# Kernel optimization log

Hardware: AMD Instinct MI355X
Metric: run time of the kernel (lower is better)

Reference implementation:

```python
import jax, jax.numpy as jnp
import numpy as np

NUM_HEADS = 16
LN_EPS = 1e-5


def setup_inputs() -> dict:
    key = jax.random.key(0)
    ks = jax.random.split(key, 5)
    B, S, H = 32768, 3, 1024
    scale = 1.0 / np.sqrt(H)
    return {
        "slots": jax.random.normal(ks[0], (B, S, H), dtype=jnp.float32),
        "in_proj_w": jax.random.normal(ks[1], (3 * H, H), dtype=jnp.float32) * scale,
        "in_proj_b": jax.random.normal(ks[2], (3 * H,), dtype=jnp.float32) * 0.02,
        "out_w": jax.random.normal(ks[3], (H, H), dtype=jnp.float32) * scale,
        "out_b": jax.random.normal(ks[4], (H,), dtype=jnp.float32) * 0.02,
        "ln_g": jnp.ones((H,), dtype=jnp.float32),
        "ln_b": jnp.zeros((H,), dtype=jnp.float32),
    }


def reference(slots, in_proj_w, in_proj_b, out_w, out_b, ln_g, ln_b):
    # slots: [B, 3, H]. Matches torch nn.MultiheadAttention (batch_first) in eval
    # mode (dropout inactive) followed by residual add + LayerNorm.
    B, S, H = slots.shape
    nh = NUM_HEADS
    dh = H // nh

    # fused QKV projection: torch does x @ in_proj_w.T + in_proj_b
    qkv = jnp.einsum("bsh,eh->bse", slots, in_proj_w) + in_proj_b  # [B,S,3H]
    q, k, v = jnp.split(qkv, 3, axis=-1)

    def heads(t):  # [B,S,H] -> [B,nh,S,dh]
        return t.reshape(B, S, nh, dh).transpose(0, 2, 1, 3)

    q, k, v = heads(q), heads(k), heads(v)

    scores = jnp.einsum("bnqd,bnkd->bnqk", q, k) / jnp.sqrt(jnp.asarray(dh, slots.dtype))
    attn = jax.nn.softmax(scores, axis=-1)  # [B,nh,3,3]
    ctx = jnp.einsum("bnqk,bnkd->bnqd", attn, v)  # [B,nh,3,dh]
    ctx = ctx.transpose(0, 2, 1, 3).reshape(B, S, H)

    attn_out = jnp.einsum("bsh,oh->bso", ctx, out_w) + out_b  # out_proj

    # residual + LayerNorm (dropout is identity at inference)
    y = slots + attn_out
    mu = jnp.mean(y, axis=-1, keepdims=True)
    var = jnp.mean(jnp.square(y - mu), axis=-1, keepdims=True)
    return (y - mu) / jnp.sqrt(var + LN_EPS) * ln_g + ln_b
```

## Files before the change

### kernel.cpp

```cpp
#include <hip/hip_runtime.h>
#include <stdint.h>

typedef unsigned short u16;
typedef float f32x4 __attribute__((ext_vector_type(4)));
typedef short bf16x8 __attribute__((ext_vector_type(8)));

__device__ __forceinline__ u16 f2bu(float f) {
  uint32_t x = __builtin_bit_cast(uint32_t, f);
  x += 0x7fffu + ((x >> 16) & 1u);
  return (u16)(x >> 16);
}
__device__ __forceinline__ float b2f(u16 u) {
  return __builtin_bit_cast(float, (uint32_t)u << 16);
}
__device__ __forceinline__ void gll16(const void* g, void* l) {
  __builtin_amdgcn_global_load_lds(
      (const __attribute__((address_space(1))) void*)g,
      (__attribute__((address_space(3))) void*)l, 16, 0, 0);
}
#define MEMFENCE asm volatile("" ::: "memory")
#define BAR() do { __builtin_amdgcn_s_barrier(); MEMFENCE; } while (0)

__global__ __launch_bounds__(256) void cvt_f32_bf16_kernel(
    const float* __restrict__ in, u16* __restrict__ out, int n4) {
  int i = blockIdx.x * 256 + threadIdx.x;
  const int stride = gridDim.x * 256;
  for (; i < n4; i += stride) {
    float4 f = reinterpret_cast<const float4*>(in)[i];
    ushort4 o;
    o.x = f2bu(f.x); o.y = f2bu(f.y); o.z = f2bu(f.z); o.w = f2bu(f.w);
    reinterpret_cast<ushort4*>(out)[i] = o;
  }
}

__global__ __launch_bounds__(512, 2) void gemm256_bt_bias(
    const u16* __restrict__ A, const u16* __restrict__ Bw,
    const float* __restrict__ bias, u16* __restrict__ C,
    int N, int K, int ntn) {
  __shared__ u16 lds[2][2][2][8192];
  const int tid = threadIdx.x;
  const int lane = tid & 63, wid = tid >> 6;
  const int wr = wid >> 2, wc = wid & 3;
  const int fr = lane & 15, kg = lane >> 4;

  const int cpx = (int)gridDim.x >> 3;
  const int bid = blockIdx.x;
  const int sid = (bid & 7) * cpx + (bid >> 3);
  const int mt = sid / ntn, nt = sid % ntn;

  const int srow = tid >> 2;
  const int scol = (tid & 3) ^ ((tid >> 3) & 3);
  const u16* Ag = A + (size_t)(mt * 256 + srow) * K + scol * 8;
  const u16* Bg = Bw + (size_t)(nt * 256 + srow) * K + scol * 8;
  const size_t rstep = (size_t)128 * K;

  const int sw = (fr >> 1) & 3;
  const int kgs = (kg ^ sw) * 8;
  const int aoff = (wr * 128 + fr) * 32 + kgs;
  const int boff = (wc * 64 + fr) * 32 + kgs;

  f32x4 acc[8][4];
#pragma unroll
  for (int i = 0; i < 8; i++)
#pragma unroll
    for (int j = 0; j < 4; j++) acc[i][j] = f32x4{0.f, 0.f, 0.f, 0.f};

  const int NT = K >> 6;

#define STAGE_A(kh, kt, nb) do {                               \
    const u16* s_ = Ag + (size_t)(kt) * 64 + (kh) * 32;        \
    gll16(s_,         &lds[nb][0][kh][wid * 512]);             \
    gll16(s_ + rstep, &lds[nb][0][kh][4096 + wid * 512]);      \
  } while (0)
#define STAGE_B(kh, kt, nb) do {                               \
    const u16* s_ = Bg + (size_t)(kt) * 64 + (kh) * 32;        \
    gll16(s_,         &lds[nb][1][kh][wid * 512]);             \
    gll16(s_ + rstep, &lds[nb][1][kh][4096 + wid * 512]);      \
  } while (0)

  STAGE_A(0, 0, 0); STAGE_B(0, 0, 0);
  STAGE_A(1, 0, 0); STAGE_B(1, 0, 0);
  asm volatile("s_waitcnt vmcnt(4)" ::: "memory");
  BAR();

  for (int t = 0; t < NT; t++) {
    const int buf = t & 1, nb = buf ^ 1;
    const bool st = (t + 1 < NT);
    const u16* As0 = &lds[buf][0][0][0];
    const u16* As1 = &lds[buf][0][1][0];
    const u16* Bs0 = &lds[buf][1][0][0];
    const u16* Bs1 = &lds[buf][1][1][0];

    bf16x8 av[8], bv[2];

#pragma unroll
    for (int mi = 0; mi < 8; mi++)
      av[mi] = *(const bf16x8*)&As0[aoff + mi * 512];
    bv[0] = *(const bf16x8*)&Bs0[boff];
    bv[1] = *(const bf16x8*)&Bs0[boff + 512];
    if (st) STAGE_A(0, t + 1, nb);
    BAR();
    __builtin_amdgcn_s_setprio(1);
#pragma unroll
    for (int mi = 0; mi < 8; mi++) {
      acc[mi][0] = __builtin_amdgcn_mfma_f32_16x16x32_bf16(av[mi], bv[0], acc[mi][0], 0, 0, 0);
      acc[mi][1] = __builtin_amdgcn_mfma_f32_16x16x32_bf16(av[mi], bv[1], acc[mi][1], 0, 0, 0);
    }
    __builtin_amdgcn_s_setprio(0);
    BAR();

    bv[0] = *(const bf16x8*)&Bs0[boff + 1024];
    bv[1] = *(const bf16x8*)&Bs0[boff + 1536];
    if (st) STAGE_B(0, t + 1, nb);
    BAR();
    __builtin_amdgcn_s_setprio(1);
#pragma unroll
    for (int mi = 0; mi < 8; mi++) {
      acc[mi][2] = __builtin_amdgcn_mfma_f32_16x16x32_bf16(av[mi], bv[0], acc[mi][2], 0, 0, 0);
      acc[mi][3] = __builtin_amdgcn_mfma_f32_16x16x32_bf16(av[mi], bv[1], acc[mi][3], 0, 0, 0);
    }
    __builtin_amdgcn_s_setprio(0);
    if (t == NT - 1) asm volatile("s_waitcnt vmcnt(0)" ::: "memory");
    else             asm volatile("s_waitcnt vmcnt(4)" ::: "memory");
    BAR();

#pragma unroll
    for (int mi = 0; mi < 8; mi++)
      av[mi] = *(const bf16x8*)&As1[aoff + mi * 512];
    bv[0] = *(const bf16x8*)&Bs1[boff];
    bv[1] = *(const bf16x8*)&Bs1[boff + 512];
    if (st) STAGE_A(1, t + 1, nb);
    BAR();
    __builtin_amdgcn_s_setprio(1);
#pragma unroll
    for (int mi = 0; mi < 8; mi++) {
      acc[mi][0] = __builtin_amdgcn_mfma_f32_16x16x32_bf16(av[mi], bv[0], acc[mi][0], 0, 0, 0);
      acc[mi][1] = __builtin_amdgcn_mfma_f32_16x16x32_bf16(av[mi], bv[1], acc[mi][1], 0, 0, 0);
    }
    __builtin_amdgcn_s_setprio(0);
    BAR();

    bv[0] = *(const bf16x8*)&Bs1[boff + 1024];
    bv[1] = *(const bf16x8*)&Bs1[boff + 1536];
    if (st) STAGE_B(1, t + 1, nb);
    BAR();
    __builtin_amdgcn_s_setprio(1);
#pragma unroll
    for (int mi = 0; mi < 8; mi++) {
      acc[mi][2] = __builtin_amdgcn_mfma_f32_16x16x32_bf16(av[mi], bv[0], acc[mi][2], 0, 0, 0);
      acc[mi][3] = __builtin_amdgcn_mfma_f32_16x16x32_bf16(av[mi], bv[1], acc[mi][3], 0, 0, 0);
    }
    __builtin_amdgcn_s_setprio(0);
    asm volatile("s_waitcnt vmcnt(4)" ::: "memory");
    BAR();
  }
#undef STAGE_A
#undef STAGE_B

  const int crow0 = mt * 256 + wr * 128 + kg * 4;
  const int ccol0 = nt * 256 + wc * 64 + fr;
#pragma unroll
  for (int nj = 0; nj < 4; nj++) {
    const int col = ccol0 + nj * 16;
    const float bb = bias[col];
#pragma unroll
    for (int mi = 0; mi < 8; mi++) {
      const int r0 = crow0 + mi * 16;
      f32x4 v = acc[mi][nj];
#pragma unroll
      for (int r = 0; r < 4; r++)
        C[(size_t)(r0 + r) * N + col] = f2bu(v[r] + bb);
    }
  }
}

__global__ __launch_bounds__(256) void attn3_kernel(
    const u16* __restrict__ qkv, u16* __restrict__ ctx) {
  const int tid = threadIdx.x;
  const int lane = tid & 63, wid = tid >> 6;
  const int unit = blockIdx.x * 4 + wid;
  const int b = unit >> 2, hg = unit & 3;
  const size_t qbase = (size_t)b * 3 * 3072 + hg * 256 + lane * 4;

  float q[3][4], k[3][4], v[3][4];
#pragma unroll
  for (int s = 0; s < 3; s++) {
    ushort4 uq = *(const ushort4*)(qkv + qbase + (size_t)s * 3072);
    ushort4 uk = *(const ushort4*)(qkv + qbase + (size_t)s * 3072 + 1024);
    ushort4 uv = *(const ushort4*)(qkv + qbase + (size_t)s * 3072 + 2048);
    q[s][0] = b2f(uq.x); q[s][1] = b2f(uq.y); q[s][2] = b2f(uq.z); q[s][3] = b2f(uq.w);
    k[s][0] = b2f(uk.x); k[s][1] = b2f(uk.y); k[s][2] = b2f(uk.z); k[s][3] = b2f(uk.w);
    v[s][0] = b2f(uv.x); v[s][1] = b2f(uv.y); v[s][2] = b2f(uv.z); v[s][3] = b2f(uv.w);
  }

  float sc[3][3];
#pragma unroll
  for (int i = 0; i < 3; i++)
#pragma unroll
    for (int j = 0; j < 3; j++) {
      float p = q[i][0] * k[j][0] + q[i][1] * k[j][1] +
                q[i][2] * k[j][2] + q[i][3] * k[j][3];
      p += __shfl_xor(p, 1);
      p += __shfl_xor(p, 2);
      p += __shfl_xor(p, 4);
      p += __shfl_xor(p, 8);
      sc[i][j] = p;
    }

  float o[3][4];
#pragma unroll
  for (int i = 0; i < 3; i++) {
    float mx = fmaxf(sc[i][0], fmaxf(sc[i][1], sc[i][2]));
    float e0 = __expf((sc[i][0] - mx) * 0.125f);
    float e1 = __expf((sc[i][1] - mx) * 0.125f);
    float e2 = __expf((sc[i][2] - mx) * 0.125f);
    float inv = 1.f / (e0 + e1 + e2);
    e0 *= inv; e1 *= inv; e2 *= inv;
#pragma unroll
    for (int d = 0; d < 4; d++)
      o[i][d] = e0 * v[0][d] + e1 * v[1][d] + e2 * v[2][d];
  }

  const size_t obase = (size_t)b * 3 * 1024 + hg * 256 + lane * 4;
#pragma unroll
  for (int i = 0; i < 3; i++) {
    ushort4 ov;
    ov.x = f2bu(o[i][0]); ov.y = f2bu(o[i][1]);
    ov.z = f2bu(o[i][2]); ov.w = f2bu(o[i][3]);
    *(ushort4*)(ctx + obase + (size_t)i * 1024) = ov;
  }
}

__global__ __launch_bounds__(256) void ln_kernel(
    const float* __restrict__ slots, const u16* __restrict__ ao,
    const float* __restrict__ g, const float* __restrict__ bvec,
    float* __restrict__ out) {
  const int tid = threadIdx.x;
  const int lane = tid & 63, wid = tid >> 6;
  const int row = blockIdx.x * 4 + wid;
  const size_t rb = (size_t)row * 1024;

  float y[16];
  float sum = 0.f, sq = 0.f;
#pragma unroll
  for (int c = 0; c < 4; c++) {
    const int col = c * 256 + lane * 4;
    float4 sl = *(const float4*)(slots + rb + col);
    ushort4 a4 = *(const ushort4*)(ao + rb + col);
    float y0 = sl.x + b2f(a4.x), y1 = sl.y + b2f(a4.y);
    float y2 = sl.z + b2f(a4.z), y3 = sl.w + b2f(a4.w);
    y[c * 4 + 0] = y0; y[c * 4 + 1] = y1; y[c * 4 + 2] = y2; y[c * 4 + 3] = y3;
    sum += y0 + y1 + y2 + y3;
    sq += y0 * y0 + y1 * y1 + y2 * y2 + y3 * y3;
  }
#pragma unroll
  for (int m = 1; m < 64; m <<= 1) {
    sum += __shfl_xor(sum, m);
    sq  += __shfl_xor(sq, m);
  }
  const float mu = sum * (1.0f / 1024.0f);
  const float var = sq * (1.0f / 1024.0f) - mu * mu;
  const float rs = rsqrtf(var + 1e-5f);
#pragma unroll
  for (int c = 0; c < 4; c++) {
    const int col = c * 256 + lane * 4;
    float4 gg = *(const float4*)(g + col);
    float4 bb = *(const float4*)(bvec + col);
    float4 ov;
    ov.x = (y[c * 4 + 0] - mu) * rs * gg.x + bb.x;
    ov.y = (y[c * 4 + 1] - mu) * rs * gg.y + bb.y;
    ov.z = (y[c * 4 + 2] - mu) * rs * gg.z + bb.z;
    ov.w = (y[c * 4 + 3] - mu) * rs * gg.w + bb.w;
    *(float4*)(out + rb + col) = ov;
  }
}

extern "C" void kernel_launch(void* const* d_in, const int* in_sizes, int n_in,
                              void* d_out, int out_size, void* d_ws, size_t ws_size,
                              hipStream_t stream) {
  const float* slots = (const float*)d_in[0];
  const float* in_w  = (const float*)d_in[1];
  const float* in_b  = (const float*)d_in[2];
  const float* out_w = (const float*)d_in[3];
  const float* out_b = (const float*)d_in[4];
  const float* ln_g  = (const float*)d_in[5];
  const float* ln_b  = (const float*)d_in[6];
  float* out = (float*)d_out;

  const int M = 32768 * 3;

  char* ws = (char*)d_ws;
  u16* Abf   = (u16*)ws;
  u16* Winb  = (u16*)(ws + 201326592);
  u16* Woutb = (u16*)(ws + 207618048);
  u16* qkv   = (u16*)(ws + 209715200);

  cvt_f32_bf16_kernel<<<2048, 256, 0, stream>>>(slots, Abf, M * 1024 / 4);
  cvt_f32_bf16_kernel<<<2048, 256, 0, stream>>>(in_w, Winb, 3072 * 1024 / 4);
  cvt_f32_bf16_kernel<<<1024, 256, 0, stream>>>(out_w, Woutb, 1024 * 1024 / 4);

  gemm256_bt_bias<<<384 * 12, 512, 0, stream>>>(Abf, Winb, in_b, qkv, 3072, 1024, 12);

  attn3_kernel<<<32768, 256, 0, stream>>>(qkv, Abf);

  gemm256_bt_bias<<<384 * 4, 512, 0, stream>>>(Abf, Woutb, out_b, qkv, 1024, 1024, 4);

  ln_kernel<<<M / 4, 256, 0, stream>>>(slots, qkv, ln_g, ln_b, out);
}
```

Measured before the change: 1.360 ms.

## Fuse out-projection GEMM with residual add and LayerNorm; grid-stride attention

Replaces the output-projection GEMM plus separate LayerNorm kernel with one kernel whose 128-row tile spans all 1024 output columns. This lets each block add bias and residual, reduce row statistics across waves through shared memory, and write normalized fp32 output directly. It removes the bf16 round-trip of the attention output and a separate LN pass. The trade-offs are a single-buffered K loop, heavy accumulator register use (limited to one block per CU), and uncoalesced strided slot/out accesses in the epilogue. The attention kernel also switches to a grid-stride loop with fewer blocks.

```diff
diff --git a/kernel.cpp b/kernel.cpp
--- a/kernel.cpp
+++ b/kernel.cpp
@@ -174,104 +174,177 @@
   }
 }
 
+__global__ __launch_bounds__(512, 1) void gemm_ln_kernel(
+    const u16* __restrict__ A,
+    const u16* __restrict__ Bw,
+    const float* __restrict__ bias,
+    const float* __restrict__ slots,
+    const float* __restrict__ g, const float* __restrict__ lnb,
+    float* __restrict__ out) {
+  __shared__ u16 As[4096];
+  __shared__ u16 Bs[32768];
+  __shared__ float red[8][128][2];
+  const int tid = threadIdx.x;
+  const int lane = tid & 63, wid = tid >> 6;
+  const int fr = lane & 15, kg = lane >> 4;
+  const int K = 1024;
+
+  const int bid = blockIdx.x;
+  const int mt = (bid & 7) * 96 + (bid >> 3);
+  const int brow = mt * 128;
+
+  const int scol = (tid & 3) ^ ((tid >> 3) & 3);
+  const u16* Ag = A + (size_t)(brow + (tid >> 2)) * K + scol * 8;
+  const u16* Bg = Bw + (size_t)(tid >> 2) * K + scol * 8;
+
+  const int sw = (fr >> 1) & 3;
+  const int kgs = (kg ^ sw) * 8;
+  const int aoff = fr * 32 + kgs;
+  const int boff = (wid * 128 + fr) * 32 + kgs;
+
+  f32x4 acc[8][8];
+#pragma unroll
+  for (int i = 0; i < 8; i++)
+#pragma unroll
+    for (int j = 0; j < 8; j++) acc[i][j] = f32x4{0.f, 0.f, 0.f, 0.f};
+
+  for (int kt = 0; kt < 32; kt++) {
+    gll16(Ag + kt * 32, &As[wid * 512]);
+#pragma unroll
+    for (int j = 0; j < 8; j++)
+      gll16(Bg + (size_t)j * 128 * K + kt * 32, &Bs[j * 4096 + wid * 512]);
+    __syncthreads();
+
+    bf16x8 af[8], bf[8];
+#pragma unroll
+    for (int mi = 0; mi < 8; mi++)
+      af[mi] = *(const bf16x8*)&As[aoff + mi * 512];
+#pragma unroll
+    for (int nj = 0; nj < 8; nj++)
+      bf[nj] = *(const bf16x8*)&Bs[boff + nj * 512];
+    __builtin_amdgcn_s_setprio(1);
+#pragma unroll
+    for (int mi = 0; mi < 8; mi++)
+#pragma unroll
+      for (int nj = 0; nj < 8; nj++)
+        acc[mi][nj] = __builtin_amdgcn_mfma_f32_16x16x32_bf16(
+            af[mi], bf[nj], acc[mi][nj], 0, 0, 0);
+    __builtin_amdgcn_s_setprio(0);
+    __syncthreads();
+  }
+
+  float bb[8], gg[8], lb[8];
+#pragma unroll
+  for (int nj = 0; nj < 8; nj++) {
+    const int col = wid * 128 + nj * 16 + fr;
+    bb[nj] = bias[col]; gg[nj] = g[col]; lb[nj] = lnb[col];
+  }
+
+#pragma unroll
+  for (int mi = 0; mi < 8; mi++)
+#pragma unroll
+    for (int r = 0; r < 4; r++) {
+      const int rl = mi * 16 + kg * 4 + r;
+      const size_t gr = (size_t)(brow + rl) * 1024;
+      float s = 0.f, q = 0.f;
+#pragma unroll
+      for (int nj = 0; nj < 8; nj++) {
+        const int col = wid * 128 + nj * 16 + fr;
+        float y = acc[mi][nj][r] + bb[nj] + slots[gr + col];
+        acc[mi][nj][r] = y;
+        s += y; q += y * y;
+      }
+#pragma unroll
+      for (int m = 1; m < 16; m <<= 1) {
+        s += __shfl_xor(s, m);
+        q += __shfl_xor(q, m);
+      }
+      if (fr == 0) { red[wid][rl][0] = s; red[wid][rl][1] = q; }
+    }
+  __syncthreads();
+
+  if (tid < 128) {
+    float s = 0.f, q = 0.f;
+#pragma unroll
+    for (int w = 0; w < 8; w++) { s += red[w][tid][0]; q += red[w][tid][1]; }
+    const float mu = s * (1.0f / 1024.0f);
+    const float var = q * (1.0f / 1024.0f) - mu * mu;
+    red[0][tid][0] = mu;
+    red[0][tid][1] = rsqrtf(var + 1e-5f);
+  }
+  __syncthreads();
+
+#pragma unroll
+  for (int mi = 0; mi < 8; mi++)
+#pragma unroll
+    for (int r = 0; r < 4; r++) {
+      const int rl = mi * 16 + kg * 4 + r;
+      const float mu = red[0][rl][0], rs = red[0][rl][1];
+      const size_t gr = (size_t)(brow + rl) * 1024;
+#pragma unroll
+      for (int nj = 0; nj < 8; nj++) {
+        const int col = wid * 128 + nj * 16 + fr;
+        out[gr + col] = (acc[mi][nj][r] - mu) * rs * gg[nj] + lb[nj];
+      }
+    }
+}
+
 __global__ __launch_bounds__(256) void attn3_kernel(
     const u16* __restrict__ qkv, u16* __restrict__ ctx) {
   const int tid = threadIdx.x;
   const int lane = tid & 63, wid = tid >> 6;
-  const int unit = blockIdx.x * 4 + wid;
-  const int b = unit >> 2, hg = unit & 3;
-  const size_t qbase = (size_t)b * 3 * 3072 + hg * 256 + lane * 4;
-
-  float q[3][4], k[3][4], v[3][4];
-#pragma unroll
-  for (int s = 0; s < 3; s++) {
-    ushort4 uq = *(const ushort4*)(qkv + qbase + (size_t)s * 3072);
-    ushort4 uk = *(const ushort4*)(qkv + qbase + (size_t)s * 3072 + 1024);
-    ushort4 uv = *(const ushort4*)(qkv + qbase + (size_t)s * 3072 + 2048);
-    q[s][0] = b2f(uq.x); q[s][1] = b2f(uq.y); q[s][2] = b2f(uq.z); q[s][3] = b2f(uq.w);
-    k[s][0] = b2f(uk.x); k[s][1] = b2f(uk.y); k[s][2] = b2f(uk.z); k[s][3] = b2f(uk.w);
-    v[s][0] = b2f(uv.x); v[s][1] = b2f(uv.y); v[s][2] = b2f(uv.z); v[s][3] = b2f(uv.w);
-  }
-
-  float sc[3][3];
-#pragma unroll
-  for (int i = 0; i < 3; i++)
-#pragma unroll
-    for (int j = 0; j < 3; j++) {
-      float p = q[i][0] * k[j][0] + q[i][1] * k[j][1] +
-                q[i][2] * k[j][2] + q[i][3] * k[j][3];
-      p += __shfl_xor(p, 1);
-      p += __shfl_xor(p, 2);
-      p += __shfl_xor(p, 4);
-      p += __shfl_xor(p, 8);
-      sc[i][j] = p;
-    }
-
-  float o[3][4];
-#pragma unroll
-  for (int i = 0; i < 3; i++) {
-    float mx = fmaxf(sc[i][0], fmaxf(sc[i][1], sc[i][2]));
-    float e0 = __expf((sc[i][0] - mx) * 0.125f);
-    float e1 = __expf((sc[i][1] - mx) * 0.125f);
-    float e2 = __expf((sc[i][2] - mx) * 0.125f);
-    float inv = 1.f / (e0 + e1 + e2);
-    e0 *= inv; e1 *= inv; e2 *= inv;
-#pragma unroll
-    for (int d = 0; d < 4; d++)
-      o[i][d] = e0 * v[0][d] + e1 * v[1][d] + e2 * v[2][d];
-  }
-
-  const size_t obase = (size_t)b * 3 * 1024 + hg * 256 + lane * 4;
-#pragma unroll
-  for (int i = 0; i < 3; i++) {
-    ushort4 ov;
-    ov.x = f2bu(o[i][0]); ov.y = f2bu(o[i][1]);
-    ov.z = f2bu(o[i][2]); ov.w = f2bu(o[i][3]);
-    *(ushort4*)(ctx + obase + (size_t)i * 1024) = ov;
-  }
-}
-
-__global__ __launch_bounds__(256) void ln_kernel(
-    const float* __restrict__ slots, const u16* __restrict__ ao,
-    const float* __restrict__ g, const float* __restrict__ bvec,
-    float* __restrict__ out) {
-  const int tid = threadIdx.x;
-  const int lane = tid & 63, wid = tid >> 6;
-  const int row = blockIdx.x * 4 + wid;
-  const size_t rb = (size_t)row * 1024;
-
-  float y[16];
-  float sum = 0.f, sq = 0.f;
-#pragma unroll
-  for (int c = 0; c < 4; c++) {
-    const int col = c * 256 + lane * 4;
-    float4 sl = *(const float4*)(slots + rb + col);
-    ushort4 a4 = *(const ushort4*)(ao + rb + col);
-    float y0 = sl.x + b2f(a4.x), y1 = sl.y + b2f(a4.y);
-    float y2 = sl.z + b2f(a4.z), y3 = sl.w + b2f(a4.w);
-    y[c * 4 + 0] = y0; y[c * 4 + 1] = y1; y[c * 4 + 2] = y2; y[c * 4 + 3] = y3;
-    sum += y0 + y1 + y2 + y3;
-    sq += y0 * y0 + y1 * y1 + y2 * y2 + y3 * y3;
-  }
-#pragma unroll
-  for (int m = 1; m < 64; m <<= 1) {
-    sum += __shfl_xor(sum, m);
-    sq  += __shfl_xor(sq, m);
-  }
-  const float mu = sum * (1.0f / 1024.0f);
-  const float var = sq * (1.0f / 1024.0f) - mu * mu;
-  const float rs = rsqrtf(var + 1e-5f);
-#pragma unroll
-  for (int c = 0; c < 4; c++) {
-    const int col = c * 256 + lane * 4;
-    float4 gg = *(const float4*)(g + col);
-    float4 bb = *(const float4*)(bvec + col);
-    float4 ov;
-    ov.x = (y[c * 4 + 0] - mu) * rs * gg.x + bb.x;
-    ov.y = (y[c * 4 + 1] - mu) * rs * gg.y + bb.y;
-    ov.z = (y[c * 4 + 2] - mu) * rs * gg.z + bb.z;
-    ov.w = (y[c * 4 + 3] - mu) * rs * gg.w + bb.w;
-    *(float4*)(out + rb + col) = ov;
+  const int nunit = 32768 * 4;
+  for (int unit = blockIdx.x * 4 + wid; unit < nunit; unit += gridDim.x * 4) {
+    const int b = unit >> 2, hg = unit & 3;
+    const size_t qbase = (size_t)b * 3 * 3072 + hg * 256 + lane * 4;
+
+    float q[3][4], k[3][4], v[3][4];
+#pragma unroll
+    for (int s = 0; s < 3; s++) {
+      ushort4 uq = *(const ushort4*)(qkv + qbase + (size_t)s * 3072);
+      ushort4 uk = *(const ushort4*)(qkv + qbase + (size_t)s * 3072 + 1024);
+      ushort4 uv = *(const ushort4*)(qkv + qbase + (size_t)s * 3072 + 2048);
+      q[s][0] = b2f(uq.x); q[s][1] = b2f(uq.y); q[s][2] = b2f(uq.z); q[s][3] = b2f(uq.w);
+      k[s][0] = b2f(uk.x); k[s][1] = b2f(uk.y); k[s][2] = b2f(uk.z); k[s][3] = b2f(uk.w);
+      v[s][0] = b2f(uv.x); v[s][1] = b2f(uv.y); v[s][2] = b2f(uv.z); v[s][3] = b2f(uv.w);
+    }
+
+    float sc[3][3];
+#pragma unroll
+    for (int i = 0; i < 3; i++)
+#pragma unroll
+      for (int j = 0; j < 3; j++) {
+        float p = q[i][0] * k[j][0] + q[i][1] * k[j][1] +
+                  q[i][2] * k[j][2] + q[i][3] * k[j][3];
+        p += __shfl_xor(p, 1);
+        p += __shfl_xor(p, 2);
+        p += __shfl_xor(p, 4);
+        p += __shfl_xor(p, 8);
+        sc[i][j] = p;
+      }
+
+    float o[3][4];
+#pragma unroll
+    for (int i = 0; i < 3; i++) {
+      float mx = fmaxf(sc[i][0], fmaxf(sc[i][1], sc[i][2]));
+      float e0 = __expf((sc[i][0] - mx) * 0.125f);
+      float e1 = __expf((sc[i][1] - mx) * 0.125f);
+      float e2 = __expf((sc[i][2] - mx) * 0.125f);
+      float inv = 1.f / (e0 + e1 + e2);
+      e0 *= inv; e1 *= inv; e2 *= inv;
+#pragma unroll
+      for (int d = 0; d < 4; d++)
+        o[i][d] = e0 * v[0][d] + e1 * v[1][d] + e2 * v[2][d];
+    }
+
+    const size_t obase = (size_t)b * 3 * 1024 + hg * 256 + lane * 4;
+#pragma unroll
+    for (int i = 0; i < 3; i++) {
+      ushort4 ov;
+      ov.x = f2bu(o[i][0]); ov.y = f2bu(o[i][1]);
+      ov.z = f2bu(o[i][2]); ov.w = f2bu(o[i][3]);
+      *(ushort4*)(ctx + obase + (size_t)i * 1024) = ov;
+    }
   }
 }
 
@@ -301,9 +374,7 @@
 
   gemm256_bt_bias<<<384 * 12, 512, 0, stream>>>(Abf, Winb, in_b, qkv, 3072, 1024, 12);
 
-  attn3_kernel<<<32768, 256, 0, stream>>>(qkv, Abf);
-
-  gemm256_bt_bias<<<384 * 4, 512, 0, stream>>>(Abf, Woutb, out_b, qkv, 1024, 1024, 4);
-
-  ln_kernel<<<M / 4, 256, 0, stream>>>(slots, qkv, ln_g, ln_b, out);
-}
+  attn3_kernel<<<2048, 256, 0, stream>>>(qkv, Abf);
+
+  gemm_ln_kernel<<<768, 512, 0, stream>>>(Abf, Woutb, out_b, slots, ln_g, ln_b, out);
+}
```

Result: slower. 2.872 ms (+111.2%).
